# Kernel tuning notes

Hardware: AMD Instinct MI355X
Metric: run time of the kernel (lower is better)

## Reference

```python
import jax, jax.numpy as jnp
import numpy as np

CAMS, HEADS, PTS, LAYERS = 6, 8, 2, 3
D, DH, FFN = 256, 32, 512
VZ, VH, VW = 8, 50, 50
NQ = VZ * VH * VW
IN_C = 768
IMG_H, IMG_W = 256, 704
FH, FW = IMG_H // 32, IMG_W // 32   # 8, 22
L = FH * FW                         # 176 tokens per camera
LVIS = 44                           # visible tokens (mask_ratio=0.75)


def _layer_norm(x, g, b, eps=1e-5):
    m = x.mean(-1, keepdims=True)
    v = x.var(-1, keepdims=True)
    return (x - m) / jnp.sqrt(v + eps) * g + b


def _group_norm(x, g, b, groups=16, eps=1e-5):
    B, C = x.shape[0], x.shape[1]
    xg = x.reshape(B, groups, C // groups, *x.shape[2:])
    m = xg.mean(axis=(2, 3, 4, 5), keepdims=True)
    v = xg.var(axis=(2, 3, 4, 5), keepdims=True)
    xg = (xg - m) / jnp.sqrt(v + eps)
    return xg.reshape(x.shape) * g[None, :, None, None, None] + b[None, :, None, None, None]


def _bilinear(val, loc, Hf, Wf):
    # val: [C, HW, heads, dh]; loc: [C, NQ, heads, P, 2] as (x, y) pixel coords
    x, y = loc[..., 0], loc[..., 1]
    x0 = jnp.floor(x); y0 = jnp.floor(y)
    wx, wy = x - x0, y - y0
    x0i, y0i = x0.astype(jnp.int32), y0.astype(jnp.int32)
    cidx = jnp.arange(val.shape[0])[:, None, None, None]
    hidx = jnp.arange(val.shape[2])[None, None, :, None]

    def g(yi, xi):
        idx = jnp.clip(yi, 0, Hf - 1) * Wf + jnp.clip(xi, 0, Wf - 1)
        return val[cidx, idx, hidx]  # [C,NQ,heads,P,dh]

    out = ((1 - wx) * (1 - wy))[..., None] * g(y0i, x0i)
    out = out + (wx * (1 - wy))[..., None] * g(y0i, x0i + 1)
    out = out + ((1 - wx) * wy)[..., None] * g(y0i + 1, x0i)
    out = out + (wx * wy)[..., None] * g(y0i + 1, x0i + 1)
    return out


def setup_inputs() -> dict:
    key = jax.random.key(0)
    ks = iter(jax.random.split(key, 48))

    def rn(shape, s=0.02):
        return jax.random.normal(next(ks), shape, jnp.float32) * s

    return {
        'camera_x': jax.random.normal(next(ks), (CAMS, LVIS, IN_C), jnp.float32),
        'camera_ids_restore': jax.random.randint(next(ks), (CAMS, L), 0, L),
        'img_h': IMG_H, 'img_w': IMG_W,
        'mask_token': rn((1, 1, IN_C)),
        'vol_emb': rn((NQ, D), 1.0),
        'W_tc': rn((D, IN_C)), 'b_tc': jnp.zeros((D,), jnp.float32),
        'cams_embeds': rn((CAMS, D), 1.0),
        'level_embeds': rn((1, D), 1.0),
        'W_off': rn((LAYERS, D, HEADS * CAMS * PTS * 2)),
        'b_off': rn((LAYERS, HEADS * CAMS * PTS * 2), 2.0),
        'W_att': rn((LAYERS, D, HEADS * CAMS * PTS)),
        'b_att': jnp.zeros((LAYERS, HEADS * CAMS * PTS), jnp.float32),
        'W_val': rn((LAYERS, D, D)), 'b_val': jnp.zeros((LAYERS, D), jnp.float32),
        'W_out': rn((LAYERS, D, D)), 'b_out': jnp.zeros((LAYERS, D), jnp.float32),
        'ln1_g': jnp.ones((LAYERS, D), jnp.float32), 'ln1_b': jnp.zeros((LAYERS, D), jnp.float32),
        'W_ff1': rn((LAYERS, D, FFN)), 'b_ff1': jnp.zeros((LAYERS, FFN), jnp.float32),
        'W_ff2': rn((LAYERS, FFN, D)), 'b_ff2': jnp.zeros((LAYERS, D), jnp.float32),
        'ln2_g': jnp.ones((LAYERS, D), jnp.float32), 'ln2_b': jnp.zeros((LAYERS, D), jnp.float32),
        'deconv_w': rn((D, D, 2, 2, 2)),
        'gn1_g': jnp.ones((D,), jnp.float32), 'gn1_b': jnp.zeros((D,), jnp.float32),
        'conv3_w': rn((192, D, 3, 3, 3)),
        'gn2_g': jnp.ones((192,), jnp.float32), 'gn2_b': jnp.zeros((192,), jnp.float32),
    }


def _forward(camera_x, camera_ids_restore, img_h, img_w, mask_token, vol_emb, W_tc, b_tc,
             cams_embeds, level_embeds, W_off, b_off, W_att, b_att, W_val, b_val, W_out, b_out,
             ln1_g, ln1_b, W_ff1, b_ff1, W_ff2, b_ff2, ln2_g, ln2_b,
             deconv_w, gn1_g, gn1_b, conv3_w, gn2_g, gn2_b):
    N, Lfull = camera_ids_restore.shape
    # 1) MAE unshuffle: append mask tokens, gather back to original order
    mt = jnp.broadcast_to(mask_token, (N, Lfull - camera_x.shape[1], IN_C)).astype(camera_x.dtype)
    full = jnp.concatenate([camera_x, mt], axis=1)                         # [N,L,C]
    full = jnp.take_along_axis(full, camera_ids_restore[:, :, None], axis=1)
    Hf, Wf = img_h // 32, img_w // 32
    cam_x = jnp.transpose(full, (0, 2, 1)).reshape(1, N, IN_C, Hf, Wf)     # [1,6,768,8,22]
    # 2) 1x1 transfer conv + ReLU
    vf = jax.nn.relu(jnp.einsum('bnchw,oc->bnohw', cam_x, W_tc) + b_tc[None, None, :, None, None])
    # 3) flatten spatial + cam/level embeds -> per-camera feature maps [N,HW,D]
    vf = jnp.transpose(vf.reshape(1, N, D, Hf * Wf), (1, 0, 3, 2))          # [N,1,HW,D]
    vf = vf + cams_embeds[:, None, None, :] + level_embeds[None, None, 0:1, :]
    feat = vf[:, 0]                                                         # [N,HW,D]
    # 4) reference points of volume queries (z slow, h, w fast) -> pixel coords
    ww = (jnp.arange(VW, dtype=jnp.float32) + 0.5) / VW
    hh = (jnp.arange(VH, dtype=jnp.float32) + 0.5) / VH
    grid = jnp.stack([jnp.tile(ww, VH), jnp.repeat(hh, VW)], axis=-1)       # [VH*VW,2]
    ref_pix = jnp.tile(grid, (VZ, 1)) * jnp.array([Wf, Hf], jnp.float32) - 0.5  # [NQ,2]
    # 5) deformable cross-attention volume encoder
    q = vol_emb
    for l in range(LAYERS):
        off = (q @ W_off[l] + b_off[l]).reshape(NQ, HEADS, CAMS, PTS, 2)
        att = jax.nn.softmax((q @ W_att[l] + b_att[l]).reshape(NQ, HEADS, CAMS * PTS), axis=-1)
        att = jnp.transpose(att.reshape(NQ, HEADS, CAMS, PTS), (2, 0, 1, 3))      # [C,NQ,H,P]
        val = (feat @ W_val[l] + b_val[l]).reshape(CAMS, Hf * Wf, HEADS, DH)
        loc = jnp.transpose(ref_pix[:, None, None, None, :] + off, (2, 0, 1, 3, 4))  # [C,NQ,H,P,2]
        sampled = _bilinear(val, loc, Hf, Wf)                                     # [C,NQ,H,P,DH]
        agg = jnp.einsum('cnhp,cnhpd->nhd', att, sampled).reshape(NQ, D)
        q = _layer_norm(q + agg @ W_out[l] + b_out[l], ln1_g[l], ln1_b[l])
        q = _layer_norm(q + jax.nn.relu(q @ W_ff1[l] + b_ff1[l]) @ W_ff2[l] + b_ff2[l], ln2_g[l], ln2_b[l])
    # 6) reshape -> [1, D, VW, VH, VZ] (matches .permute(0,4,3,2,1))
    vol = jnp.transpose(q.reshape(1, VZ, VH, VW, D), (0, 4, 3, 2, 1))
    # 7) deblock: deconv3d(k=2,s=2) -> GN16 -> ReLU -> conv3d(k=3,p=1) -> GN16 -> ReLU
    x = jax.lax.conv_transpose(vol, deconv_w, (2, 2, 2), 'VALID',
                               dimension_numbers=('NCDHW', 'OIDHW', 'NCDHW'))
    x = jax.nn.relu(_group_norm(x, gn1_g, gn1_b))
    x = jax.lax.conv_general_dilated(x, conv3_w, (1, 1, 1), [(1, 1)] * 3,
                                     dimension_numbers=('NCDHW', 'OIDHW', 'NCDHW'))
    x = jax.nn.relu(_group_norm(x, gn2_g, gn2_b))
    return x, cam_x


def reference(camera_x, camera_ids_restore, img_h, img_w, mask_token, vol_emb, W_tc, b_tc,
              cams_embeds, level_embeds, W_off, b_off, W_att, b_att, W_val, b_val, W_out, b_out,
              ln1_g, ln1_b, W_ff1, b_ff1, W_ff2, b_ff2, ln2_g, ln2_b,
              deconv_w, gn1_g, gn1_b, conv3_w, gn2_g, gn2_b):
    return _forward(camera_x, camera_ids_restore, img_h, img_w, mask_token, vol_emb, W_tc, b_tc,
                    cams_embeds, level_embeds, W_off, b_off, W_att, b_att, W_val, b_val, W_out, b_out,
                    ln1_g, ln1_b, W_ff1, b_ff1, W_ff2, b_ff2, ln2_g, ln2_b,
                    deconv_w, gn1_g, gn1_b, conv3_w, gn2_g, gn2_b)
```

## Files before the change

kernel.cpp:

```cpp
#include <hip/hip_runtime.h>
#include <stdint.h>

typedef __attribute__((ext_vector_type(8))) short s16x8;
typedef __attribute__((ext_vector_type(4))) float f32x4;

static __device__ __forceinline__ unsigned short f2bf(float f) {
  unsigned u = __float_as_uint(f);
  u += 0x7FFFu + ((u >> 16) & 1u);
  return (unsigned short)(u >> 16);
}
static __device__ __forceinline__ float bf2f(unsigned short h) {
  return __uint_as_float(((unsigned)h) << 16);
}
static __device__ __forceinline__ void sum8(uint4 u, float& a, float& q) {
  unsigned w[4] = {u.x, u.y, u.z, u.w};
#pragma unroll
  for (int i = 0; i < 4; ++i) {
    float v0 = __uint_as_float((w[i] & 0xFFFFu) << 16);
    float v1 = __uint_as_float(w[i] & 0xFFFF0000u);
    a += v0 + v1;
    q += v0 * v0 + v1 * v1;
  }
}

__global__ void k_prep(const float* __restrict__ W_tc, const float* __restrict__ W_val,
                       const float* __restrict__ W_off, const float* __restrict__ W_att,
                       const float* __restrict__ W_out, const float* __restrict__ W_ff1,
                       const float* __restrict__ W_ff2, const float* __restrict__ deconv_w,
                       const float* __restrict__ conv3_w,
                       unsigned short* __restrict__ Wt_tc, unsigned short* __restrict__ Wt_val,
                       unsigned short* __restrict__ Wt_oa, unsigned short* __restrict__ Wt_out,
                       unsigned short* __restrict__ Wt_ff1, unsigned short* __restrict__ Wt_ff2,
                       unsigned short* __restrict__ Wt_dc, unsigned short* __restrict__ wc3) {
  int idx = blockIdx.x * 256 + threadIdx.x;
  if (idx < 196608) { Wt_tc[idx] = f2bf(W_tc[idx]); return; }
  idx -= 196608;
  if (idx < 196608) {
    int l = idx / 65536, r = idx - l * 65536, k = r >> 8, n = r & 255;
    Wt_val[l * 65536 + n * 256 + k] = f2bf(W_val[l * 65536 + r]);
    return;
  }
  idx -= 196608;
  if (idx < 147456) {
    int l = idx / 49152, r = idx - l * 49152, k = r / 192, n = r - k * 192;
    Wt_oa[l * 73728 + n * 256 + k] = f2bf(W_off[l * 49152 + r]);
    return;
  }
  idx -= 147456;
  if (idx < 73728) {
    int l = idx / 24576, r = idx - l * 24576, k = r / 96, n = r - k * 96;
    Wt_oa[l * 73728 + 192 * 256 + n * 256 + k] = f2bf(W_att[l * 24576 + r]);
    return;
  }
  idx -= 73728;
  if (idx < 196608) {
    int l = idx / 65536, r = idx - l * 65536, k = r >> 8, n = r & 255;
    Wt_out[l * 65536 + n * 256 + k] = f2bf(W_out[l * 65536 + r]);
    return;
  }
  idx -= 196608;
  if (idx < 393216) {
    int l = idx / 131072, r = idx - l * 131072, k = r >> 9, n = r & 511;
    Wt_ff1[l * 131072 + n * 256 + k] = f2bf(W_ff1[l * 131072 + r]);
    return;
  }
  idx -= 393216;
  if (idx < 393216) {
    int l = idx / 131072, r = idx - l * 131072, k = r >> 8, n = r & 255;
    Wt_ff2[l * 131072 + n * 512 + k] = f2bf(W_ff2[l * 131072 + r]);
    return;
  }
  idx -= 393216;
  if (idx < 524288) {
    int n = idx >> 8, k = idx & 255;
    Wt_dc[idx] = f2bf(deconv_w[(size_t)(n & 255) * 2048 + k * 8 + (n >> 8)]);
    return;
  }
  idx -= 524288;
  if (idx < 1327104) {
    int tap = idx / 49152;
    int rem = idx - tap * 49152;
    int oc = rem >> 8, ic = rem & 255;
    int chunk = ic >> 5, kg = (ic >> 3) & 3, j = ic & 7;
    int ocblk = oc >> 4, lo = oc & 15;
    size_t frag = (size_t)(tap * 8 + chunk) * 12 + ocblk;
    wc3[(frag * 64 + kg * 16 + lo) * 8 + j] = f2bf(conv3_w[(oc * 256 + ic) * 27 + tap]);
    return;
  }
}

__global__ void k_cvt(const float* __restrict__ in, unsigned short* __restrict__ out, int n) {
  int i = blockIdx.x * 256 + threadIdx.x;
  if (i < n) out[i] = f2bf(in[i]);
}

__global__ void k_restore2(const float* __restrict__ cx, const int* __restrict__ ids,
                           const float* __restrict__ mtok, float* __restrict__ out_camx,
                           unsigned short* __restrict__ camxT) {
  int idx = blockIdx.x * 256 + threadIdx.x;
  if (idx >= 811008) return;
  int ch = idx % 768;
  int row = idx / 768;
  int c = row / 176, p = row - c * 176;
  int id = ids[c * 176 + p];
  float v = (id < 44) ? cx[((size_t)(c * 44 + id)) * 768 + ch] : mtok[ch];
  camxT[idx] = f2bf(v);
  out_camx[((size_t)(c * 768 + ch)) * 176 + p] = v;
}

template <int MODE>
__global__ __launch_bounds__(256) void k_gemm(
    const unsigned short* __restrict__ A, int M, int lda,
    const unsigned short* __restrict__ Bt, int K, int N,
    const float* __restrict__ bias, const float* __restrict__ bias2, int n1, int relu,
    float* __restrict__ Cf, unsigned short* __restrict__ Cb, int ldc,
    const float* __restrict__ cemb, const float* __restrict__ lemb) {
  __shared__ short sA[128 * 40];
  const int t = threadIdx.x;
  const int l = t & 63, w = t >> 6;
  const int lo = l & 15, kg = l >> 4;
  const int row0 = blockIdx.x * 128, n0 = blockIdx.y * 64;
  const s16x8 bz = {0, 0, 0, 0, 0, 0, 0, 0};
  f32x4 acc[2][4] = {};
  s16x8 bc[4], bn[4];
#pragma unroll
  for (int nb = 0; nb < 4; ++nb) {
    int n = n0 + nb * 16 + lo;
    bc[nb] = (n < N) ? *(const s16x8*)&Bt[(size_t)n * K + kg * 8] : bz;
  }
  const int stR = t >> 1, stH = t & 1;
  for (int kc = 0; kc < K; kc += 32) {
    const bool pf = (kc + 32 < K);
    if (pf) {
#pragma unroll
      for (int nb = 0; nb < 4; ++nb) {
        int n = n0 + nb * 16 + lo;
        bn[nb] = (n < N) ? *(const s16x8*)&Bt[(size_t)n * K + kc + 32 + kg * 8] : bz;
      }
    }
    __syncthreads();
    {
      int r = row0 + stR;
      uint4 v0 = {0u, 0u, 0u, 0u}, v1 = {0u, 0u, 0u, 0u};
      if (r < M) {
        const unsigned short* src = A + (size_t)r * lda + kc + stH * 16;
        v0 = *(const uint4*)src;
        v1 = *(const uint4*)(src + 8);
      }
      *(uint4*)&sA[stR * 40 + stH * 16] = v0;
      *(uint4*)&sA[stR * 40 + stH * 16 + 8] = v1;
    }
    __syncthreads();
    s16x8 a0 = *(const s16x8*)&sA[(w * 32 + lo) * 40 + kg * 8];
    s16x8 a1 = *(const s16x8*)&sA[(w * 32 + 16 + lo) * 40 + kg * 8];
#pragma unroll
    for (int nb = 0; nb < 4; ++nb) {
      acc[0][nb] = __builtin_amdgcn_mfma_f32_16x16x32_bf16(a0, bc[nb], acc[0][nb], 0, 0, 0);
      acc[1][nb] = __builtin_amdgcn_mfma_f32_16x16x32_bf16(a1, bc[nb], acc[1][nb], 0, 0, 0);
    }
    if (pf) {
#pragma unroll
      for (int nb = 0; nb < 4; ++nb) bc[nb] = bn[nb];
    }
  }
#pragma unroll
  for (int m = 0; m < 2; ++m)
#pragma unroll
    for (int nb = 0; nb < 4; ++nb)
#pragma unroll
      for (int r = 0; r < 4; ++r) {
        int row = row0 + w * 32 + m * 16 + (kg << 2) + r;
        int col = n0 + nb * 16 + lo;
        if (row < M && col < N) {
          float v = acc[m][nb][r];
          if (bias) v += (col < n1) ? bias[col] : bias2[col - n1];
          if (relu) v = fmaxf(v, 0.f);
          if (MODE == 0) {
            Cf[(size_t)row * ldc + col] = v;
          } else if (MODE == 2) {
            Cb[(size_t)row * ldc + col] = f2bf(v);
          } else {
            v += cemb[(row / 176) * 256 + col] + lemb[col];
            Cb[(size_t)row * ldc + col] = f2bf(v);
          }
        }
      }
}

__global__ __launch_bounds__(256, 2) void k_deconv(const unsigned short* __restrict__ A,
                                                   const unsigned short* __restrict__ Bt,
                                                   unsigned short* __restrict__ Cb, int M) {
  __shared__ short sA[128 * 256];
  const int t = threadIdx.x;
  const int l = t & 63, w = t >> 6;
  const int lo = l & 15, kg = l >> 4;
  const int row0 = blockIdx.x * 128;
#pragma unroll
  for (int i = 0; i < 16; ++i) {
    int g = t + i * 256;
    int row = g >> 5, gcol = g & 31;
    int r = row0 + row;
    uint4 v = {0u, 0u, 0u, 0u};
    if (r < M) v = *(const uint4*)&A[(size_t)r * 256 + gcol * 8];
    *(uint4*)&sA[row * 256 + ((gcol ^ (row & 7)) << 3)] = v;
  }
  __syncthreads();
  const int r0 = w * 32 + lo, r1 = r0 + 16;
  for (int nt = 0; nt < 32; ++nt) {
    f32x4 acc[2][4] = {};
    s16x8 bc[4], bn[4];
    const int ncol0 = nt * 64;
#pragma unroll
    for (int nb = 0; nb < 4; ++nb)
      bc[nb] = *(const s16x8*)&Bt[(size_t)(ncol0 + nb * 16 + lo) * 256 + kg * 8];
#pragma unroll
    for (int kc = 0; kc < 8; ++kc) {
      const bool pf = kc < 7;
      if (pf) {
#pragma unroll
        for (int nb = 0; nb < 4; ++nb)
          bn[nb] = *(const s16x8*)&Bt[(size_t)(ncol0 + nb * 16 + lo) * 256 + (kc + 1) * 32 + kg * 8];
      }
      int g0 = kc * 4 + kg;
      s16x8 a0 = *(const s16x8*)&sA[r0 * 256 + ((g0 ^ (r0 & 7)) << 3)];
      s16x8 a1 = *(const s16x8*)&sA[r1 * 256 + ((g0 ^ (r1 & 7)) << 3)];
#pragma unroll
      for (int nb = 0; nb < 4; ++nb) {
        acc[0][nb] = __builtin_amdgcn_mfma_f32_16x16x32_bf16(a0, bc[nb], acc[0][nb], 0, 0, 0);
        acc[1][nb] = __builtin_amdgcn_mfma_f32_16x16x32_bf16(a1, bc[nb], acc[1][nb], 0, 0, 0);
      }
      if (pf) {
#pragma unroll
        for (int nb = 0; nb < 4; ++nb) bc[nb] = bn[nb];
      }
    }
    const int tap = nt >> 2;
    const int t1 = tap >> 2, t2 = (tap >> 1) & 1, t3 = tap & 1;
#pragma unroll
    for (int m = 0; m < 2; ++m)
#pragma unroll
      for (int nb = 0; nb < 4; ++nb)
#pragma unroll
        for (int r = 0; r < 4; ++r) {
          int row = row0 + w * 32 + m * 16 + (kg << 2) + r;
          if (row < M) {
            int oc = (nt & 3) * 64 + nb * 16 + lo;
            int z = row / 2500, rr = row - z * 2500;
            int hy = rr / 50, wx = rr - hy * 50;
            int od = 2 * wx + 1 - t1, oh = 2 * hy + 1 - t2, ow = 2 * z + 1 - t3;
            Cb[((size_t)((od * 100 + oh) * 16 + ow)) * 256 + oc] = f2bf(acc[m][nb][r]);
          }
        }
  }
}

__global__ __launch_bounds__(256) void k_sample(const float* __restrict__ oa,
                                                const float* __restrict__ val,
                                                unsigned short* __restrict__ aggb) {
  __shared__ float sl[96], sw[96];
  int t = threadIdx.x;
  int h = t >> 5, d = t & 31;
  const float* vbh0 = val + (size_t)h * 32 + d;
  for (int r = 0; r < 8; ++r) {
    int n = blockIdx.x * 8 + r;
    if (t < 96) sl[t] = oa[(size_t)n * 288 + 192 + t];
    __syncthreads();
    if (t < 96) {
      int hh = t / 12;
      float mx = -1e30f;
#pragma unroll
      for (int j = 0; j < 12; ++j) mx = fmaxf(mx, sl[hh * 12 + j]);
      sw[t] = __expf(sl[t] - mx);
    }
    __syncthreads();
    float ssum = 0.f;
#pragma unroll
    for (int j = 0; j < 12; ++j) ssum += sw[h * 12 + j];
    float inv = 1.f / ssum;
    float xr = ((float)(n % 50) + 0.5f) * (22.0f / 50.0f) - 0.5f;
    float yr = ((float)((n / 50) % 50) + 0.5f) * (8.0f / 50.0f) - 0.5f;
    float acc = 0.f;
    const float* offn = oa + (size_t)n * 288 + h * 24;
#pragma unroll
    for (int c = 0; c < 6; ++c)
#pragma unroll
      for (int p2 = 0; p2 < 2; ++p2) {
        float x = xr + offn[(c * 2 + p2) * 2];
        float y = yr + offn[(c * 2 + p2) * 2 + 1];
        float x0 = floorf(x), y0 = floorf(y);
        float wx = x - x0, wy = y - y0;
        int ix0 = min(max((int)x0, 0), 21), ix1 = min(max((int)x0 + 1, 0), 21);
        int iy0 = min(max((int)y0, 0), 7), iy1 = min(max((int)y0 + 1, 0), 7);
        const float* vb = vbh0 + (size_t)c * 176 * 768;
        float v00 = vb[(size_t)(iy0 * 22 + ix0) * 768];
        float v01 = vb[(size_t)(iy0 * 22 + ix1) * 768];
        float v10 = vb[(size_t)(iy1 * 22 + ix0) * 768];
        float v11 = vb[(size_t)(iy1 * 22 + ix1) * 768];
        float bil = (1.f - wx) * (1.f - wy) * v00 + wx * (1.f - wy) * v01 +
                    (1.f - wx) * wy * v10 + wx * wy * v11;
        acc += sw[h * 12 + c * 2 + p2] * inv * bil;
      }
    aggb[(size_t)n * 256 + t] = f2bf(acc);
    __syncthreads();
  }
}

__global__ __launch_bounds__(256) void k_addln(unsigned short* __restrict__ qb,
                                               const unsigned short* __restrict__ p,
                                               const float* __restrict__ g, const float* __restrict__ b) {
  __shared__ float red[8];
  int t = threadIdx.x;
  int w = t >> 6;
  float gg = g[t], bb = b[t];
  for (int r = 0; r < 8; ++r) {
    size_t n = (size_t)blockIdx.x * 8 + r;
    float x = bf2f(qb[n * 256 + t]) + bf2f(p[n * 256 + t]);
    float s1 = x, s2 = x * x;
#pragma unroll
    for (int o = 32; o >= 1; o >>= 1) {
      s1 += __shfl_xor(s1, o, 64);
      s2 += __shfl_xor(s2, o, 64);
    }
    if ((t & 63) == 0) { red[w * 2] = s1; red[w * 2 + 1] = s2; }
    __syncthreads();
    s1 = red[0] + red[2] + red[4] + red[6];
    s2 = red[1] + red[3] + red[5] + red[7];
    float mean = s1 * (1.0f / 256.0f);
    float var = s2 * (1.0f / 256.0f) - mean * mean;
    float y = (x - mean) * rsqrtf(var + 1e-5f) * gg + bb;
    qb[n * 256 + t] = f2bf(y);
    __syncthreads();
  }
}

__global__ __launch_bounds__(256) void k_gnstat1(const unsigned short* __restrict__ X, float* __restrict__ part) {
  __shared__ float s1[256], s2[256];
  int b = blockIdx.x, t = threadIdx.x;
  int oc8 = t & 31, v0 = t >> 5;
  float a = 0.f, q = 0.f;
#pragma unroll
  for (int i = 0; i < 8; ++i) {
    int vox = v0 + i * 8;
    uint4 u = *(const uint4*)&X[(size_t)b * 16384 + vox * 256 + oc8 * 8];
    sum8(u, a, q);
  }
  s1[t] = a; s2[t] = q;
  __syncthreads();
  if (t < 128) { s1[t] += s1[t + 128]; s2[t] += s2[t + 128]; }
  __syncthreads();
  if (t < 64) { s1[t] += s1[t + 64]; s2[t] += s2[t + 64]; }
  __syncthreads();
  if (t < 32) { s1[t] += s1[t + 32]; s2[t] += s2[t + 32]; }
  __syncthreads();
  if (t < 16) {
    part[t * 2500 + b] = s1[2 * t] + s1[2 * t + 1];
    part[40000 + t * 2500 + b] = s2[2 * t] + s2[2 * t + 1];
  }
}

__global__ __launch_bounds__(256) void k_gnred1(const float* __restrict__ part, float* __restrict__ gmv) {
  __shared__ float s1[256], s2[256];
  int g = blockIdx.x, t = threadIdx.x;
  float a = 0.f, q = 0.f;
  for (int i = t; i < 2500; i += 256) { a += part[g * 2500 + i]; q += part[40000 + g * 2500 + i]; }
  s1[t] = a; s2[t] = q;
  __syncthreads();
  for (int s = 128; s > 0; s >>= 1) {
    if (t < s) { s1[t] += s1[t + s]; s2[t] += s2[t + s]; }
    __syncthreads();
  }
  if (t == 0) {
    float m = s1[0] / 2560000.0f;
    float v = s2[0] / 2560000.0f - m * m;
    gmv[2 * g] = m; gmv[2 * g + 1] = rsqrtf(v + 1e-5f);
  }
}

__global__ __launch_bounds__(256) void k_gnapply1(unsigned short* __restrict__ X, const float* __restrict__ gmv,
                                                  const float* __restrict__ g, const float* __restrict__ b) {
  for (unsigned i = blockIdx.x * 256 + threadIdx.x; i < 5120000u; i += gridDim.x * 256) {
    unsigned e = i * 8u;
    int oc0 = e & 255, grp = oc0 >> 4;
    float mean = gmv[grp * 2], rstd = gmv[grp * 2 + 1];
    float4 g0 = *(const float4*)&g[oc0], g1 = *(const float4*)&g[oc0 + 4];
    float4 b0 = *(const float4*)&b[oc0], b1 = *(const float4*)&b[oc0 + 4];
    uint4 u = *(const uint4*)&X[e];
    unsigned w[4] = {u.x, u.y, u.z, u.w};
    float gg[8] = {g0.x, g0.y, g0.z, g0.w, g1.x, g1.y, g1.z, g1.w};
    float bb[8] = {b0.x, b0.y, b0.z, b0.w, b1.x, b1.y, b1.z, b1.w};
    unsigned o[4];
#pragma unroll
    for (int j = 0; j < 4; ++j) {
      float v0 = __uint_as_float((w[j] & 0xFFFFu) << 16);
      float v1 = __uint_as_float(w[j] & 0xFFFF0000u);
      v0 = fmaxf((v0 - mean) * rstd * gg[2 * j] + bb[2 * j], 0.f);
      v1 = fmaxf((v1 - mean) * rstd * gg[2 * j + 1] + bb[2 * j + 1], 0.f);
      o[j] = (unsigned)f2bf(v0) | ((unsigned)f2bf(v1) << 16);
    }
    *(uint4*)&X[e] = make_uint4(o[0], o[1], o[2], o[3]);
  }
}

__global__ __launch_bounds__(256, 2) void k_conv3(const unsigned short* __restrict__ X,
                                                  const unsigned short* __restrict__ Wp,
                                                  unsigned short* __restrict__ Y) {
  __shared__ short sX[4 * 543 * 8];
  int bid = blockIdx.x;
  int xcd = bid & 7, idx = bid >> 3;
  int swz = (xcd < 4 ? xcd * 163 : 652 + (xcd - 4) * 162) + idx;
  const int od = swz / 13;
  const int oh0 = (swz - od * 13) * 8;
  const int t = threadIdx.x;
  const int l = t & 63, w = t >> 6;
  const int kg = l >> 4, lo = l & 15;
  f32x4 acc[8][3] = {};
  s16x8 bc[9], bn[9];
  const unsigned short* Wl = Wp + (size_t)l * 8;
  const int w3 = w * 3;
#pragma unroll
  for (int t2 = 0; t2 < 3; ++t2)
#pragma unroll
    for (int nb = 0; nb < 3; ++nb)
      bc[t2 * 3 + nb] = *(const s16x8*)&Wl[(size_t)((t2 * 3 * 8) * 12 + w3 + nb) * 512];

  for (int gi = 0; gi < 72; ++gi) {
    const int chunk = gi / 9;
    const int sub = gi - chunk * 9;
    const int t1 = sub / 3, t3 = sub - t1 * 3;
    if (sub == 0) {
      __syncthreads();
#pragma unroll
      for (int i = 0; i < 9; ++i) {
        int e = t + i * 256;
        if (e < 2160) {
          int pos = e >> 2, ks = e & 3;
          int sd = pos / 180, r2 = pos - sd * 180;
          int sh = r2 / 18, sw_ = r2 - sh * 18;
          int gd = od + sd - 1, gh = oh0 + sh - 1, gw = sw_ - 1;
          uint4 v = {0u, 0u, 0u, 0u};
          if ((unsigned)gd < 100u && (unsigned)gh < 100u && (unsigned)gw < 16u)
            v = *(const uint4*)&X[((size_t)((gd * 100 + gh) * 16 + gw)) * 256 + chunk * 32 + ks * 8];
          *(uint4*)&sX[(ks * 543 + pos) * 8] = v;
        }
      }
      __syncthreads();
    }
    const int gn1 = gi + 1;
    if (gn1 < 72) {
      const int c1 = gn1 / 9, su1 = gn1 - c1 * 9;
      const int t1n = su1 / 3, t3n = su1 - t1n * 3;
#pragma unroll
      for (int t2 = 0; t2 < 3; ++t2)
#pragma unroll
        for (int nb = 0; nb < 3; ++nb)
          bn[t2 * 3 + nb] = *(const s16x8*)&Wl[
              (size_t)(((t1n * 9 + t2 * 3 + t3n) * 8 + c1) * 12 + w3 + nb) * 512];
    }
    const int abase = kg * 543 + t1 * 180 + lo + t3;
#pragma unroll
    for (int sh = 0; sh < 10; ++sh) {
      s16x8 a = *(const s16x8*)&sX[(abase + sh * 18) * 8];
#pragma unroll
      for (int t2 = 0; t2 < 3; ++t2) {
        const int m = sh - t2;
        if (m >= 0 && m < 8) {
          acc[m][0] = __builtin_amdgcn_mfma_f32_16x16x32_bf16(a, bc[t2 * 3 + 0], acc[m][0], 0, 0, 0);
          acc[m][1] = __builtin_amdgcn_mfma_f32_16x16x32_bf16(a, bc[t2 * 3 + 1], acc[m][1], 0, 0, 0);
          acc[m][2] = __builtin_amdgcn_mfma_f32_16x16x32_bf16(a, bc[t2 * 3 + 2], acc[m][2], 0, 0, 0);
        }
      }
    }
#pragma unroll
    for (int i = 0; i < 9; ++i) bc[i] = bn[i];
  }
#pragma unroll
  for (int m = 0; m < 8; ++m) {
    int oh = oh0 + m;
    if (oh < 100) {
#pragma unroll
      for (int nb = 0; nb < 3; ++nb)
#pragma unroll
        for (int r = 0; r < 4; ++r) {
          int oc = w * 48 + nb * 16 + lo;
          int ow = (kg << 2) + r;
          Y[(size_t)oc * 160000 + (size_t)((od * 100 + oh) * 16) + ow] = f2bf(acc[m][nb][r]);
        }
    }
  }
}

__global__ __launch_bounds__(256) void k_gnstat2(const unsigned short* __restrict__ X, float* __restrict__ part) {
  __shared__ float s1[256], s2[256];
  int b = blockIdx.x, t = threadIdx.x;
  int ch = b / 10, pp = b - ch * 10;
  const unsigned short* base = X + (size_t)ch * 160000 + (size_t)pp * 16000;
  float a = 0.f, q = 0.f;
  for (int i = t; i < 2000; i += 256) {
    uint4 u = *(const uint4*)&base[i * 8];
    sum8(u, a, q);
  }
  s1[t] = a; s2[t] = q;
  __syncthreads();
  for (int s = 128; s > 0; s >>= 1) {
    if (t < s) { s1[t] += s1[t + s]; s2[t] += s2[t + s]; }
    __syncthreads();
  }
  if (t == 0) { part[80000 + ch * 10 + pp] = s1[0]; part[81920 + ch * 10 + pp] = s2[0]; }
}

__global__ __launch_bounds__(256) void k_gnred2(const float* __restrict__ part, float* __restrict__ gmv) {
  __shared__ float s1[256], s2[256];
  int g = blockIdx.x, t = threadIdx.x;
  float a = (t < 120) ? part[80000 + g * 120 + t] : 0.f;
  float q = (t < 120) ? part[81920 + g * 120 + t] : 0.f;
  s1[t] = a; s2[t] = q;
  __syncthreads();
  for (int s = 128; s > 0; s >>= 1) {
    if (t < s) { s1[t] += s1[t + s]; s2[t] += s2[t + s]; }
    __syncthreads();
  }
  if (t == 0) {
    float m = s1[0] / 1920000.0f;
    float v = s2[0] / 1920000.0f - m * m;
    gmv[2 * g] = m; gmv[2 * g + 1] = rsqrtf(v + 1e-5f);
  }
}

__global__ __launch_bounds__(256) void k_gnapply2(const unsigned short* __restrict__ X, const float* __restrict__ gmv,
                                                  const float* __restrict__ g, const float* __restrict__ b,
                                                  float* __restrict__ out) {
  for (unsigned i = blockIdx.x * 256 + threadIdx.x; i < 3840000u; i += gridDim.x * 256) {
    unsigned oc = i / 20000u;
    unsigned grp = oc / 12u;
    float mean = gmv[grp * 2], rstd = gmv[grp * 2 + 1];
    float gam = g[oc], bet = b[oc];
    unsigned e = i * 8u;
    uint4 u = *(const uint4*)&X[e];
    unsigned wv[4] = {u.x, u.y, u.z, u.w};
    float o[8];
#pragma unroll
    for (int j = 0; j < 4; ++j) {
      float v0 = __uint_as_float((wv[j] & 0xFFFFu) << 16);
      float v1 = __uint_as_float(wv[j] & 0xFFFF0000u);
      o[2 * j] = fmaxf((v0 - mean) * rstd * gam + bet, 0.f);
      o[2 * j + 1] = fmaxf((v1 - mean) * rstd * gam + bet, 0.f);
    }
    *(float4*)&out[e] = make_float4(o[0], o[1], o[2], o[3]);
    *(float4*)&out[e + 4] = make_float4(o[4], o[5], o[6], o[7]);
  }
}

static inline dim3 gemm_grid(int M, int N) { return dim3((M + 127) / 128, (N + 63) / 64); }

extern "C" void kernel_launch(void* const* d_in, const int* in_sizes, int n_in,
                              void* d_out, int out_size, void* d_ws, size_t ws_size,
                              hipStream_t stream) {
  const float* camera_x = (const float*)d_in[0];
  const int* ids = (const int*)d_in[1];
  const float* mask_tok = (const float*)d_in[4];
  const float* vol_emb = (const float*)d_in[5];
  const float* W_tc = (const float*)d_in[6];
  const float* b_tc = (const float*)d_in[7];
  const float* cams_emb = (const float*)d_in[8];
  const float* lvl_emb = (const float*)d_in[9];
  const float* W_off = (const float*)d_in[10];
  const float* b_off = (const float*)d_in[11];
  const float* W_att = (const float*)d_in[12];
  const float* b_att = (const float*)d_in[13];
  const float* W_val = (const float*)d_in[14];
  const float* b_val = (const float*)d_in[15];
  const float* W_out = (const float*)d_in[16];
  const float* b_out = (const float*)d_in[17];
  const float* ln1_g = (const float*)d_in[18];
  const float* ln1_b = (const float*)d_in[19];
  const float* W_ff1 = (const float*)d_in[20];
  const float* b_ff1 = (const float*)d_in[21];
  const float* W_ff2 = (const float*)d_in[22];
  const float* b_ff2 = (const float*)d_in[23];
  const float* ln2_g = (const float*)d_in[24];
  const float* ln2_b = (const float*)d_in[25];
  const float* deconv_w = (const float*)d_in[26];
  const float* gn1_g = (const float*)d_in[27];
  const float* gn1_b = (const float*)d_in[28];
  const float* conv3_w = (const float*)d_in[29];
  const float* gn2_g = (const float*)d_in[30];
  const float* gn2_b = (const float*)d_in[31];

  char* ws = (char*)d_ws;
  unsigned short* qb   = (unsigned short*)(ws + 20480000);
  unsigned short* projb= (unsigned short*)(ws + 30720000);
  float* oa            = (float*)(ws + 51200000);
  unsigned short* aggb = (unsigned short*)(ws + 74240000);
  unsigned short* ffhb = (unsigned short*)(ws + 84480000);
  float* val3          = (float*)(ws + 104960000);
  unsigned short* featb= (unsigned short*)(ws + 108204032);
  unsigned short* x1bf = (unsigned short*)(ws + 30720000);
  unsigned short* c3   = (unsigned short*)(ws + 112640000);
  unsigned short* Wt_val = (unsigned short*)(ws + 174080000);
  unsigned short* Wt_oa  = (unsigned short*)(ws + 174473216);
  unsigned short* Wt_out = (unsigned short*)(ws + 174915584);
  unsigned short* Wt_ff1 = (unsigned short*)(ws + 175308800);
  unsigned short* Wt_ff2 = (unsigned short*)(ws + 176095232);
  unsigned short* Wt_dc  = (unsigned short*)(ws + 176881664);
  unsigned short* wc3    = (unsigned short*)(ws + 177930240);
  float* part = (float*)(ws + 180584448);
  float* gmv1 = (float*)(ws + 180920320);
  float* gmv2 = (float*)(ws + 180920448);
  unsigned short* Wt_tc  = (unsigned short*)(ws + 180920576);
  unsigned short* camxT  = (unsigned short*)(ws + 181707008);

  float* out_x = (float*)d_out;
  float* out_camx = out_x + 30720000;

  k_prep<<<13472, 256, 0, stream>>>(W_tc, W_val, W_off, W_att, W_out, W_ff1, W_ff2,
                                    deconv_w, conv3_w,
                                    Wt_tc, Wt_val, Wt_oa, Wt_out, Wt_ff1, Wt_ff2, Wt_dc, wc3);

  k_restore2<<<3168, 256, 0, stream>>>(camera_x, ids, mask_tok, out_camx, camxT);
  k_gemm<4><<<gemm_grid(1056, 256), 256, 0, stream>>>(camxT, 1056, 768, Wt_tc, 768, 256,
                                                      b_tc, nullptr, 256, 1, nullptr, featb, 256,
                                                      cams_emb, lvl_emb);
  k_cvt<<<20000, 256, 0, stream>>>(vol_emb, qb, 5120000);

  k_gemm<0><<<gemm_grid(1056, 768), 256, 0, stream>>>(featb, 1056, 256, Wt_val, 256, 768,
                                                      b_val, nullptr, 768, 0, val3, nullptr, 768,
                                                      nullptr, nullptr);

  for (int lyr = 0; lyr < 3; ++lyr) {
    k_gemm<0><<<gemm_grid(20000, 288), 256, 0, stream>>>(qb, 20000, 256, Wt_oa + lyr * 73728, 256, 288,
                                                         b_off + lyr * 192, b_att + lyr * 96, 192, 0,
                                                         oa, nullptr, 288, nullptr, nullptr);
    k_sample<<<2500, 256, 0, stream>>>(oa, val3 + lyr * 256, aggb);
    k_gemm<2><<<gemm_grid(20000, 256), 256, 0, stream>>>(aggb, 20000, 256, Wt_out + lyr * 65536, 256, 256,
                                                         b_out + lyr * 256, nullptr, 256, 0,
                                                         nullptr, projb, 256, nullptr, nullptr);
    k_addln<<<2500, 256, 0, stream>>>(qb, projb, ln1_g + lyr * 256, ln1_b + lyr * 256);
    k_gemm<2><<<gemm_grid(20000, 512), 256, 0, stream>>>(qb, 20000, 256, Wt_ff1 + lyr * 131072, 256, 512,
                                                         b_ff1 + lyr * 512, nullptr, 512, 1,
                                                         nullptr, ffhb, 512, nullptr, nullptr);
    k_gemm<2><<<gemm_grid(20000, 256), 256, 0, stream>>>(ffhb, 20000, 512, Wt_ff2 + lyr * 131072, 512, 256,
                                                         b_ff2 + lyr * 256, nullptr, 256, 0,
                                                         nullptr, projb, 256, nullptr, nullptr);
    k_addln<<<2500, 256, 0, stream>>>(qb, projb, ln2_g + lyr * 256, ln2_b + lyr * 256);
  }

  k_deconv<<<157, 256, 0, stream>>>(qb, Wt_dc, x1bf, 20000);

  k_gnstat1<<<2500, 256, 0, stream>>>(x1bf, part);
  k_gnred1<<<16, 256, 0, stream>>>(part, gmv1);
  k_gnapply1<<<2048, 256, 0, stream>>>(x1bf, gmv1, gn1_g, gn1_b);

  k_conv3<<<1300, 256, 0, stream>>>(x1bf, wc3, c3);

  k_gnstat2<<<1920, 256, 0, stream>>>(c3, part);
  k_gnred2<<<16, 256, 0, stream>>>(part, gmv2);
  k_gnapply2<<<2048, 256, 0, stream>>>(c3, gmv2, gn2_g, gn2_b, out_x);
}
```

Baseline: 1.416 ms.

## Double-buffer conv3 input tile in LDS with register prefetch of next chunk

The conv3 kernel previously stalled at each 32-channel chunk boundary to load the input halo tile into shared memory between two barriers. It now holds two LDS buffers, issues global loads for the next chunk into registers before the chunk's MFMA loop, and writes them into the alternate buffer afterwards, leaving one barrier per chunk. This is meant to hide global load latency behind compute. The cost is doubled LDS (about 35KB per block) and 36 extra VGPRs for staged data, which may reduce occupancy under launch_bounds(256,2) or cause spills.

```diff
diff --git a/kernel.cpp b/kernel.cpp
--- a/kernel.cpp
+++ b/kernel.cpp
@@ -404,7 +404,7 @@
 __global__ __launch_bounds__(256, 2) void k_conv3(const unsigned short* __restrict__ X,
                                                   const unsigned short* __restrict__ Wp,
                                                   unsigned short* __restrict__ Y) {
-  __shared__ short sX[4 * 543 * 8];
+  __shared__ short sX[2][4 * 543 * 8];
   int bid = blockIdx.x;
   int xcd = bid & 7, idx = bid >> 3;
   int swz = (xcd < 4 ? xcd * 163 : 652 + (xcd - 4) * 162) + idx;
@@ -423,55 +423,90 @@
     for (int nb = 0; nb < 3; ++nb)
       bc[t2 * 3 + nb] = *(const s16x8*)&Wl[(size_t)((t2 * 3 * 8) * 12 + w3 + nb) * 512];
 
-  for (int gi = 0; gi < 72; ++gi) {
-    const int chunk = gi / 9;
-    const int sub = gi - chunk * 9;
-    const int t1 = sub / 3, t3 = sub - t1 * 3;
-    if (sub == 0) {
-      __syncthreads();
+#pragma unroll
+  for (int i = 0; i < 9; ++i) {
+    int e = t + i * 256;
+    if (e < 2160) {
+      int pos = e >> 2, ks = e & 3;
+      int sd = pos / 180, r2 = pos - sd * 180;
+      int sh = r2 / 18, sw_ = r2 - sh * 18;
+      int gd = od + sd - 1, gh = oh0 + sh - 1, gw = sw_ - 1;
+      uint4 v = {0u, 0u, 0u, 0u};
+      if ((unsigned)gd < 100u && (unsigned)gh < 100u && (unsigned)gw < 16u)
+        v = *(const uint4*)&X[((size_t)((gd * 100 + gh) * 16 + gw)) * 256 + ks * 8];
+      *(uint4*)&sX[0][(ks * 543 + pos) * 8] = v;
+    }
+  }
+  __syncthreads();
+  int cur = 0;
+  for (int chunk = 0; chunk < 8; ++chunk) {
+    uint4 sv[9];
+    const bool pfs = (chunk < 7);
+    if (pfs) {
 #pragma unroll
       for (int i = 0; i < 9; ++i) {
         int e = t + i * 256;
+        uint4 v = {0u, 0u, 0u, 0u};
         if (e < 2160) {
           int pos = e >> 2, ks = e & 3;
           int sd = pos / 180, r2 = pos - sd * 180;
           int sh = r2 / 18, sw_ = r2 - sh * 18;
           int gd = od + sd - 1, gh = oh0 + sh - 1, gw = sw_ - 1;
-          uint4 v = {0u, 0u, 0u, 0u};
           if ((unsigned)gd < 100u && (unsigned)gh < 100u && (unsigned)gw < 16u)
-            v = *(const uint4*)&X[((size_t)((gd * 100 + gh) * 16 + gw)) * 256 + chunk * 32 + ks * 8];
-          *(uint4*)&sX[(ks * 543 + pos) * 8] = v;
+            v = *(const uint4*)&X[((size_t)((gd * 100 + gh) * 16 + gw)) * 256 + (chunk + 1) * 32 + ks * 8];
         }
-      }
-      __syncthreads();
-    }
-    const int gn1 = gi + 1;
-    if (gn1 < 72) {
-      const int c1 = gn1 / 9, su1 = gn1 - c1 * 9;
-      const int t1n = su1 / 3, t3n = su1 - t1n * 3;
-#pragma unroll
-      for (int t2 = 0; t2 < 3; ++t2)
-#pragma unroll
-        for (int nb = 0; nb < 3; ++nb)
-          bn[t2 * 3 + nb] = *(const s16x8*)&Wl[
-              (size_t)(((t1n * 9 + t2 * 3 + t3n) * 8 + c1) * 12 + w3 + nb) * 512];
-    }
-    const int abase = kg * 543 + t1 * 180 + lo + t3;
-#pragma unroll
-    for (int sh = 0; sh < 10; ++sh) {
-      s16x8 a = *(const s16x8*)&sX[(abase + sh * 18) * 8];
-#pragma unroll
-      for (int t2 = 0; t2 < 3; ++t2) {
-        const int m = sh - t2;
-        if (m >= 0 && m < 8) {
-          acc[m][0] = __builtin_amdgcn_mfma_f32_16x16x32_bf16(a, bc[t2 * 3 + 0], acc[m][0], 0, 0, 0);
-          acc[m][1] = __builtin_amdgcn_mfma_f32_16x16x32_bf16(a, bc[t2 * 3 + 1], acc[m][1], 0, 0, 0);
-          acc[m][2] = __builtin_amdgcn_mfma_f32_16x16x32_bf16(a, bc[t2 * 3 + 2], acc[m][2], 0, 0, 0);
+        sv[i] = v;
+      }
+    }
+#pragma unroll
+    for (int sub = 0; sub < 9; ++sub) {
+      const int t1 = sub / 3, t3 = sub - t1 * 3;
+      if (sub < 8) {
+        const int su1 = sub + 1;
+        const int t1n = su1 / 3, t3n = su1 - t1n * 3;
+#pragma unroll
+        for (int t2 = 0; t2 < 3; ++t2)
+#pragma unroll
+          for (int nb = 0; nb < 3; ++nb)
+            bn[t2 * 3 + nb] = *(const s16x8*)&Wl[
+                (size_t)(((t1n * 9 + t2 * 3 + t3n) * 8 + chunk) * 12 + w3 + nb) * 512];
+      } else if (pfs) {
+#pragma unroll
+        for (int t2 = 0; t2 < 3; ++t2)
+#pragma unroll
+          for (int nb = 0; nb < 3; ++nb)
+            bn[t2 * 3 + nb] = *(const s16x8*)&Wl[
+                (size_t)(((t2 * 3 * 8) + chunk + 1) * 12 + w3 + nb) * 512];
+      }
+      const int abase = kg * 543 + t1 * 180 + lo + t3;
+#pragma unroll
+      for (int sh = 0; sh < 10; ++sh) {
+        s16x8 a = *(const s16x8*)&sX[cur][(abase + sh * 18) * 8];
+#pragma unroll
+        for (int t2 = 0; t2 < 3; ++t2) {
+          const int m = sh - t2;
+          if (m >= 0 && m < 8) {
+            acc[m][0] = __builtin_amdgcn_mfma_f32_16x16x32_bf16(a, bc[t2 * 3 + 0], acc[m][0], 0, 0, 0);
+            acc[m][1] = __builtin_amdgcn_mfma_f32_16x16x32_bf16(a, bc[t2 * 3 + 1], acc[m][1], 0, 0, 0);
+            acc[m][2] = __builtin_amdgcn_mfma_f32_16x16x32_bf16(a, bc[t2 * 3 + 2], acc[m][2], 0, 0, 0);
+          }
         }
       }
-    }
-#pragma unroll
-    for (int i = 0; i < 9; ++i) bc[i] = bn[i];
+#pragma unroll
+      for (int i = 0; i < 9; ++i) bc[i] = bn[i];
+    }
+    if (pfs) {
+#pragma unroll
+      for (int i = 0; i < 9; ++i) {
+        int e = t + i * 256;
+        if (e < 2160) {
+          int pos = e >> 2, ks = e & 3;
+          *(uint4*)&sX[cur ^ 1][(ks * 543 + pos) * 8] = sv[i];
+        }
+      }
+      cur ^= 1;
+    }
+    __syncthreads();
   }
 #pragma unroll
   for (int m = 0; m < 8; ++m) {
```

After: 1.440 ms. No clear change (+1.7%).
